# Performance work log

Measured on AMD Instinct MI355X. Metric: run time of the kernel, lower is better.

Reference implementation:

```python
import jax, jax.numpy as jnp
import numpy as np

TEMPERATURE = 0.05


def _hungarian_max(C):
    """Jonker-Volgenant shortest-augmenting-path LAP on a square numpy matrix.
    Returns col index matched to each row, maximizing total cost
    (equivalent to scipy.optimize.linear_sum_assignment(C, maximize=True))."""
    cost = -np.asarray(C, dtype=np.float64)  # minimize negated cost
    n = cost.shape[0]
    INF = np.inf
    u = np.zeros(n + 1)
    v = np.zeros(n + 1)
    p = np.zeros(n + 1, dtype=np.int64)   # p[j] = row matched to column j (1-based)
    way = np.zeros(n + 1, dtype=np.int64)
    for i in range(1, n + 1):
        p[0] = i
        j0 = 0
        minv = np.full(n + 1, INF)
        used = np.zeros(n + 1, dtype=bool)
        while True:
            used[j0] = True
            i0 = p[j0]
            delta = INF
            j1 = -1
            for j in range(1, n + 1):
                if not used[j]:
                    cur = cost[i0 - 1, j - 1] - u[i0] - v[j]
                    if cur < minv[j]:
                        minv[j] = cur
                        way[j] = j0
                    if minv[j] < delta:
                        delta = minv[j]
                        j1 = j
            for j in range(n + 1):
                if used[j]:
                    u[p[j]] += delta
                    v[j] -= delta
                else:
                    minv[j] -= delta
            j0 = j1
            if p[j0] == 0:
                break
        while j0:
            j1 = way[j0]
            p[j0] = p[j1]
            j0 = j1
    col_of_row = np.zeros(n, dtype=np.int64)
    for j in range(1, n + 1):
        col_of_row[p[j] - 1] = j - 1
    return col_of_row


def setup_inputs() -> dict:
    key = jax.random.key(0)
    k1, k2, k3 = jax.random.split(key, 3)
    B, K, D = 256, 16, 1024
    return {
        "outputs": jax.random.normal(k1, (B, K, D), dtype=jnp.float32),
        "positive_embeddings": jax.random.normal(k2, (B, K, D), dtype=jnp.float32),
        "negative_embeddings": jax.random.normal(k3, (B, K, D), dtype=jnp.float32),
    }


def reference(outputs, positive_embeddings, negative_embeddings):
    B, K, D = outputs.shape
    o = outputs.reshape(B * K, D) / TEMPERATURE          # (BK, D)
    emb = jnp.concatenate(
        [positive_embeddings.reshape(B * K, D),
         negative_embeddings.reshape(B * K, D)], axis=0)  # (2BK, D)
    sim = jnp.einsum("bd,cd->bc", o, emb)                 # (BK, 2BK)
    sim = jax.nn.log_softmax(sim, axis=1)
    # i-th KxK diagonal block: rows [K*i, K*(i+1)), cols [K*i, K*(i+1))
    idx = jnp.arange(B)
    blocks = sim.reshape(B, K, 2 * B, K)[idx, :, idx, :]  # (B, K, K)
    # Hungarian matching (detached in original -> no grad through assignment)
    blk_np = np.asarray(jax.device_get(jax.lax.stop_gradient(blocks)))
    cols = jnp.asarray(np.stack([_hungarian_max(blk_np[b]) for b in range(B)]))  # (B, K)
    matched = blocks[idx[:, None], jnp.arange(K)[None, :], cols]  # (B, K)
    # per-sample mean of -matched, then mean over batch == overall mean
    return jnp.mean(-matched)
```

## Files before the change

### kernel.cpp

```cpp
#include <hip/hip_runtime.h>
#include <hip/hip_bf16.h>
#include <math.h>

#define Ddim 1024
#define Mrows 4096
#define Ncols 8192
#define BM 128
#define BN 128
#define BK 32
#define NCS 64
#define CS 64
#define RT (Mrows / BM)
#define KITERS (Ddim / BK)
#define SCALE 20.0f
#define ARR_ELEMS (Mrows * Ddim)

typedef __bf16 bf16_t;
typedef __bf16 bf16x8 __attribute__((ext_vector_type(8)));
typedef float f32x4 __attribute__((ext_vector_type(4)));

#define LOAD16_TO_LDS(g, l)                                                  \
  __builtin_amdgcn_global_load_lds(                                          \
      (const __attribute__((address_space(1))) void*)(g),                    \
      (__attribute__((address_space(3))) void*)(l), 16, 0, 0)

__global__ __launch_bounds__(256) void cvt_kernel(
    const float* __restrict__ o, const float* __restrict__ pos,
    const float* __restrict__ neg, bf16_t* __restrict__ ob,
    bf16_t* __restrict__ pb, bf16_t* __restrict__ nb,
    float* __restrict__ out)
{
  if (blockIdx.x == 0 && threadIdx.x == 0) out[0] = 0.f;
  const int idx = blockIdx.x * 256 + threadIdx.x;
  const int seg = idx >> 19;
  const int off = idx & ((1 << 19) - 1);
  const float* src = (seg == 0) ? o : (seg == 1) ? pos : neg;
  bf16_t* dst = (seg == 0) ? ob : (seg == 1) ? pb : nb;
  const float4 v0 = *(const float4*)(src + (size_t)off * 8);
  const float4 v1 = *(const float4*)(src + (size_t)off * 8 + 4);
  bf16x8 r = {(bf16_t)v0.x, (bf16_t)v0.y, (bf16_t)v0.z, (bf16_t)v0.w,
              (bf16_t)v1.x, (bf16_t)v1.y, (bf16_t)v1.z, (bf16_t)v1.w};
  *(bf16x8*)(dst + (size_t)off * 8) = r;
}

__global__ __launch_bounds__(256, 4) void gemm_lse_kernel(
    const bf16_t* __restrict__ ob, const bf16_t* __restrict__ pb,
    const bf16_t* __restrict__ nb, float* __restrict__ pm,
    float* __restrict__ pl, float* __restrict__ blocks_raw)
{
  __shared__ bf16_t As[2][BM * BK];
  __shared__ bf16_t Bs[2][BN * BK];

  const int bid = blockIdx.x;
  const int rt = bid >> 6;
  const int cs = bid & 63;
  const int row0 = rt * BM;
  const bf16_t* Eb = (cs < 32) ? (pb + (size_t)cs * BN * Ddim)
                               : (nb + (size_t)(cs - 32) * BN * Ddim);

  const int t = threadIdx.x;
  const int wave = t >> 6;
  const int lane = t & 63;
  const int quad = lane >> 4;
  const int l16 = lane & 15;
  const int koff = ((quad ^ ((l16 >> 1) & 3)) << 3);
  const int lr4 = lane >> 2;
  const int cstg = lane & 3;

  f32x4 acc[2][8];
#pragma unroll
  for (int a = 0; a < 2; ++a)
#pragma unroll
    for (int b = 0; b < 8; ++b) acc[a][b] = (f32x4){0.f, 0.f, 0.f, 0.f};

#pragma unroll
  for (int cl = 0; cl < 2; ++cl) {
    const int r = wave * 32 + cl * 16 + lr4;
    const int gc = cstg ^ ((r >> 1) & 3);
    LOAD16_TO_LDS(ob + (size_t)(row0 + r) * Ddim + gc * 8,
                  &As[0][(wave * 32 + cl * 16) * BK]);
    LOAD16_TO_LDS(Eb + (size_t)r * Ddim + gc * 8,
                  &Bs[0][(wave * 32 + cl * 16) * BK]);
  }

  int p = 0;
  for (int kc = 0; kc < KITERS; ++kc) {
    __syncthreads();
    if (kc + 1 < KITERS) {
      const int k0 = (kc + 1) * BK;
#pragma unroll
      for (int cl = 0; cl < 2; ++cl) {
        const int r = wave * 32 + cl * 16 + lr4;
        const int gc = cstg ^ ((r >> 1) & 3);
        LOAD16_TO_LDS(ob + (size_t)(row0 + r) * Ddim + k0 + gc * 8,
                      &As[p ^ 1][(wave * 32 + cl * 16) * BK]);
        LOAD16_TO_LDS(Eb + (size_t)r * Ddim + k0 + gc * 8,
                      &Bs[p ^ 1][(wave * 32 + cl * 16) * BK]);
      }
    }

    const int rowA0 = wave * 32 + l16;
    const bf16x8 a0 = *(const bf16x8*)(&As[p][rowA0 * BK + koff]);
    const bf16x8 a1 = *(const bf16x8*)(&As[p][(rowA0 + 16) * BK + koff]);
#pragma unroll
    for (int fn = 0; fn < 8; ++fn) {
      const bf16x8 bf = *(const bf16x8*)(&Bs[p][(fn * 16 + l16) * BK + koff]);
      acc[0][fn] = __builtin_amdgcn_mfma_f32_16x16x32_bf16(a0, bf, acc[0][fn], 0, 0, 0);
      acc[1][fn] = __builtin_amdgcn_mfma_f32_16x16x32_bf16(a1, bf, acc[1][fn], 0, 0, 0);
    }
    p ^= 1;
  }

#pragma unroll
  for (int fm = 0; fm < 2; ++fm) {
#pragma unroll
    for (int r = 0; r < 4; ++r) {
      float s[8];
#pragma unroll
      for (int fn = 0; fn < 8; ++fn) s[fn] = acc[fm][fn][r] * SCALE;
      float m = s[0];
#pragma unroll
      for (int fn = 1; fn < 8; ++fn) m = fmaxf(m, s[fn]);
#pragma unroll
      for (int off = 1; off <= 8; off <<= 1)
        m = fmaxf(m, __shfl_xor(m, off, 64));
      float l = 0.f;
#pragma unroll
      for (int fn = 0; fn < 8; ++fn) l += __expf(s[fn] - m);
#pragma unroll
      for (int off = 1; off <= 8; off <<= 1)
        l += __shfl_xor(l, off, 64);
      if (l16 == 0) {
        const int rg = row0 + wave * 32 + fm * 16 + quad * 4 + r;
        pm[(size_t)rg * CS + cs] = m;
        pl[(size_t)rg * CS + cs] = l;
      }
    }
  }

  if (cs == rt) {
#pragma unroll
    for (int fm = 0; fm < 2; ++fm) {
      const int d = 2 * wave + fm;
      const int b = rt * 8 + d;
#pragma unroll
      for (int fn = 0; fn < 8; ++fn) {
        if (fn == d) {
#pragma unroll
          for (int r = 0; r < 4; ++r)
            blocks_raw[b * 256 + (quad * 4 + r) * 16 + l16] = acc[fm][fn][r] * SCALE;
        }
      }
    }
  }
}

__global__ __launch_bounds__(64) void hungarian_kernel(
    const float* __restrict__ blocks_raw, const float* __restrict__ pm,
    const float* __restrict__ pl, float* __restrict__ out)
{
  const int b = blockIdx.x;
  const int L = threadIdx.x;
  __shared__ float C[16][16];
  __shared__ float lse_s[16];

  for (int e = L; e < 256; e += 64)
    C[e >> 4][e & 15] = blocks_raw[b * 256 + e];

  {
    const int r = L & 15, g = L >> 4;
    const size_t base = (size_t)(b * 16 + r) * CS + g * 16;
    float m = -INFINITY, l = 0.f;
#pragma unroll
    for (int k = 0; k < 16; ++k) {
      const float m2 = pm[base + k];
      const float l2 = pl[base + k];
      const float M = fmaxf(m, m2);
      l = l * __expf(m - M) + l2 * __expf(m2 - M);
      m = M;
    }
#pragma unroll
    for (int off = 16; off <= 32; off <<= 1) {
      const float m2 = __shfl_xor(m, off, 64);
      const float l2 = __shfl_xor(l, off, 64);
      const float M = fmaxf(m, m2);
      l = l * __expf(m - M) + l2 * __expf(m2 - M);
      m = M;
    }
    if (g == 0) lse_s[r] = m + logf(l);
  }

  const float INF = 3.0e38f;
  float vj = 0.f, u_reg = 0.f;
  int pj = 0;
  float minv = INF;
  int wayj = 0;
  bool usedj = false, on_tree = false;

  for (int i = 1; i <= 16; ++i) {
    if (L == 0) pj = i;
    minv = INF; wayj = 0; usedj = false; on_tree = false;
    int j0 = 0;
    while (true) {
      usedj = usedj || (L == j0);
      const int i0 = __shfl(pj, j0, 64);
      if (L == i0) on_tree = true;
      const float ui0 = __shfl(u_reg, i0, 64);
      if (L >= 1 && L <= 16 && !usedj) {
        const float cur = -C[i0 - 1][L - 1] - ui0 - vj;
        if (cur < minv) { minv = cur; wayj = j0; }
      }
      float cand = (L >= 1 && L <= 16 && !usedj) ? minv : INF;
      int idx = L;
#pragma unroll
      for (int off = 16; off > 0; off >>= 1) {
        const float ov = __shfl_xor(cand, off, 32);
        const int oi = __shfl_xor(idx, off, 32);
        if (ov < cand || (ov == cand && oi < idx)) { cand = ov; idx = oi; }
      }
      const float delta = cand;
      const int j1 = __builtin_amdgcn_readfirstlane(idx);
      if (L >= 1 && L <= 16) {
        if (usedj) vj -= delta; else minv -= delta;
        if (on_tree) u_reg += delta;
      }
      j0 = j1;
      const int pj0 = __shfl(pj, j0, 64);
      if (pj0 == 0) break;
    }
    while (j0 != 0) {
      const int j1a = __shfl(wayj, j0, 64);
      const int pjn = __shfl(pj, j1a, 64);
      if (L == j0) pj = pjn;
      j0 = j1a;
    }
  }

  float loss = 0.f;
  if (L >= 1 && L <= 16) loss = lse_s[pj - 1] - C[pj - 1][L - 1];
#pragma unroll
  for (int off = 32; off > 0; off >>= 1) loss += __shfl_down(loss, off, 64);
  if (L == 0) atomicAdd(out, loss * (1.0f / 4096.0f));
}

extern "C" void kernel_launch(void* const* d_in, const int* in_sizes, int n_in,
                              void* d_out, int out_size, void* d_ws, size_t ws_size,
                              hipStream_t stream) {
  const float* o   = (const float*)d_in[0];
  const float* pos = (const float*)d_in[1];
  const float* neg = (const float*)d_in[2];
  float* out = (float*)d_out;

  float* ws = (float*)d_ws;
  float* pm         = ws;
  float* pl         = pm + (size_t)4096 * CS;
  float* blocks_raw = pl + (size_t)4096 * CS;
  bf16_t* ob = (bf16_t*)(blocks_raw + 65536);
  bf16_t* pb = ob + (size_t)ARR_ELEMS;
  bf16_t* nb = pb + (size_t)ARR_ELEMS;

  cvt_kernel<<<3 * ARR_ELEMS / 8 / 256, 256, 0, stream>>>(o, pos, neg, ob, pb, nb, out);
  gemm_lse_kernel<<<RT * NCS, 256, 0, stream>>>(ob, pb, nb, pm, pl, blocks_raw);
  hungarian_kernel<<<256, 64, 0, stream>>>(blocks_raw, pm, pl, out);
}
```

Measured before the change: 221.8 us.

## Keep Hungarian cost column in registers, fold row potentials, use DPP min-reduce

```diff
diff --git a/kernel.cpp b/kernel.cpp
--- a/kernel.cpp
+++ b/kernel.cpp
@@ -155,17 +155,50 @@
   }
 }
 
+__device__ __forceinline__ float select16(const float c[16], int k) {
+  float t8[8], t4[4], t2[2];
+#pragma unroll
+  for (int i = 0; i < 8; ++i) t8[i] = (k & 1) ? c[2 * i + 1] : c[2 * i];
+#pragma unroll
+  for (int i = 0; i < 4; ++i) t4[i] = (k & 2) ? t8[2 * i + 1] : t8[2 * i];
+#pragma unroll
+  for (int i = 0; i < 2; ++i) t2[i] = (k & 4) ? t4[2 * i + 1] : t4[2 * i];
+  return (k & 8) ? t2[1] : t2[0];
+}
+
+__device__ __forceinline__ float wave_min64(float x) {
+#define DPP_STEP(ctrl)                                                        \
+  {                                                                           \
+    int xi = __builtin_bit_cast(int, x);                                      \
+    int yi = __builtin_amdgcn_update_dpp(xi, xi, ctrl, 0xf, 0xf, false);      \
+    x = fminf(x, __builtin_bit_cast(float, yi));                              \
+  }
+  DPP_STEP(0x111)
+  DPP_STEP(0x112)
+  DPP_STEP(0x114)
+  DPP_STEP(0x118)
+  DPP_STEP(0x142)
+  DPP_STEP(0x143)
+#undef DPP_STEP
+  return __builtin_bit_cast(
+      float, __builtin_amdgcn_readlane(__builtin_bit_cast(int, x), 63));
+}
+
 __global__ __launch_bounds__(64) void hungarian_kernel(
     const float* __restrict__ blocks_raw, const float* __restrict__ pm,
     const float* __restrict__ pl, float* __restrict__ out)
 {
   const int b = blockIdx.x;
   const int L = threadIdx.x;
-  __shared__ float C[16][16];
   __shared__ float lse_s[16];
 
-  for (int e = L; e < 256; e += 64)
-    C[e >> 4][e & 15] = blocks_raw[b * 256 + e];
+  const int jc = (L >= 1 && L <= 16) ? (L - 1) : 0;
+  float c[16], w[16];
+#pragma unroll
+  for (int i = 0; i < 16; ++i) {
+    c[i] = blocks_raw[b * 256 + i * 16 + jc];
+    w[i] = -c[i];
+  }
 
   {
     const int r = L & 15, g = L >> 4;
@@ -191,53 +224,50 @@
   }
 
   const float INF = 3.0e38f;
-  float vj = 0.f, u_reg = 0.f;
+  float vj = 0.f;
   int pj = 0;
   float minv = INF;
   int wayj = 0;
-  bool usedj = false, on_tree = false;
+  bool usedj = false;
 
   for (int i = 1; i <= 16; ++i) {
     if (L == 0) pj = i;
-    minv = INF; wayj = 0; usedj = false; on_tree = false;
+    minv = INF; wayj = 0; usedj = false;
+    unsigned tree = 0;
     int j0 = 0;
+    int i0 = i;
     while (true) {
       usedj = usedj || (L == j0);
-      const int i0 = __shfl(pj, j0, 64);
-      if (L == i0) on_tree = true;
-      const float ui0 = __shfl(u_reg, i0, 64);
+      tree |= 1u << (i0 - 1);
+      const float wi0 = select16(w, i0 - 1);
       if (L >= 1 && L <= 16 && !usedj) {
-        const float cur = -C[i0 - 1][L - 1] - ui0 - vj;
+        const float cur = wi0 - vj;
         if (cur < minv) { minv = cur; wayj = j0; }
       }
-      float cand = (L >= 1 && L <= 16 && !usedj) ? minv : INF;
-      int idx = L;
-#pragma unroll
-      for (int off = 16; off > 0; off >>= 1) {
-        const float ov = __shfl_xor(cand, off, 32);
-        const int oi = __shfl_xor(idx, off, 32);
-        if (ov < cand || (ov == cand && oi < idx)) { cand = ov; idx = oi; }
-      }
-      const float delta = cand;
-      const int j1 = __builtin_amdgcn_readfirstlane(idx);
+      const float cand = (L >= 1 && L <= 16 && !usedj) ? minv : INF;
+      const float delta = wave_min64(cand);
+      const unsigned long long bal = __ballot(cand == delta);
+      const int j1 = (int)__builtin_ctzll(bal);
       if (L >= 1 && L <= 16) {
         if (usedj) vj -= delta; else minv -= delta;
-        if (on_tree) u_reg += delta;
-      }
+      }
+#pragma unroll
+      for (int k = 0; k < 16; ++k)
+        if (tree & (1u << k)) w[k] -= delta;
       j0 = j1;
-      const int pj0 = __shfl(pj, j0, 64);
-      if (pj0 == 0) break;
+      i0 = __builtin_amdgcn_readlane(pj, j0);
+      if (i0 == 0) break;
     }
     while (j0 != 0) {
-      const int j1a = __shfl(wayj, j0, 64);
-      const int pjn = __shfl(pj, j1a, 64);
+      const int j1a = __builtin_amdgcn_readlane(wayj, j0);
+      const int pjn = __builtin_amdgcn_readlane(pj, j1a);
       if (L == j0) pj = pjn;
       j0 = j1a;
     }
   }
 
   float loss = 0.f;
-  if (L >= 1 && L <= 16) loss = lse_s[pj - 1] - C[pj - 1][L - 1];
+  if (L >= 1 && L <= 16) loss = lse_s[pj - 1] - select16(c, pj - 1);
 #pragma unroll
   for (int off = 32; off > 0; off >>= 1) loss += __shfl_down(loss, off, 64);
   if (L == 0) atomicAdd(out, loss * (1.0f / 4096.0f));
```

New measurement: 253.9 us. +14.5%, slower.
